# Performance work log

Hardware: AMD Instinct MI355X
Metric: run time of the kernel (lower is better)

The kernel has to match this reference:

```python
import jax, jax.numpy as jnp
import numpy as np

B, C1, C2, K, H, W = 2, 256, 256, 3, 64, 64
PAD = 1
EPS = 1e-5
K2 = K * K
OUT_OFF = 3 * K2  # deform_groups=1: 2*k2 offset channels + k2 mask channels


def setup_inputs() -> dict:
    key = jax.random.key(0)
    ks = jax.random.split(key, 8)
    x = jax.random.normal(ks[0], (B, C1, H, W), jnp.float32)
    # small scale so predicted offsets stay within a few pixels (realistic trained regime)
    w_off = jax.random.normal(ks[1], (OUT_OFF, C1, 3, 3), jnp.float32) * 0.01
    b_off = jax.random.normal(ks[2], (OUT_OFF,), jnp.float32) * 0.01
    w_dcn = jax.random.normal(ks[3], (C2, C1, K, K), jnp.float32) / np.sqrt(C1 * K2).astype(np.float32)
    gamma = 1.0 + 0.1 * jax.random.normal(ks[4], (C2,), jnp.float32)
    beta = 0.1 * jax.random.normal(ks[5], (C2,), jnp.float32)
    run_mean = 0.1 * jax.random.normal(ks[6], (C2,), jnp.float32)
    run_var = jax.random.uniform(ks[7], (C2,), jnp.float32, minval=0.5, maxval=1.5)
    return {"x": x, "w_off": w_off, "b_off": b_off, "w_dcn": w_dcn,
            "gamma": gamma, "beta": beta, "run_mean": run_mean, "run_var": run_var}


def _dcnv2_bn_silu(x, w_off, b_off, w_dcn, gamma, beta, run_mean, run_var):
    # offset/mask predictor: plain 3x3 conv, stride 1, pad 1
    om = jax.lax.conv_general_dilated(x, w_off, (1, 1), [(PAD, PAD), (PAD, PAD)])
    om = om + b_off[None, :, None, None]  # [B, 27, H, W]
    # mmcv channel layout: (dy, dx) interleaved per kernel tap, then mask
    offset = om[:, :2 * K2].reshape(B, K2, 2, H, W)
    mask = jax.nn.sigmoid(om[:, 2 * K2:3 * K2])  # [B, K2, H, W]
    dy, dx = offset[:, :, 0], offset[:, :, 1]     # [B, K2, H, W]

    ki = jnp.arange(K)
    tap_y = jnp.repeat(ki, K)  # [K2]
    tap_x = jnp.tile(ki, K)    # [K2]
    base_y = jnp.arange(H)[None, None, :, None] - PAD + tap_y[None, :, None, None]
    base_x = jnp.arange(W)[None, None, None, :] - PAD + tap_x[None, :, None, None]
    py = base_y.astype(x.dtype) + dy  # [B, K2, H, W] sampling rows
    px = base_x.astype(x.dtype) + dx  # [B, K2, H, W] sampling cols

    y0f = jnp.floor(py)
    x0f = jnp.floor(px)
    ly = (py - y0f)[:, None]  # [B, 1, K2, H, W]
    lx = (px - x0f)[:, None]
    y0 = y0f.astype(jnp.int32)
    x0 = x0f.astype(jnp.int32)

    x_flat = x.reshape(B, C1, H * W)

    def gather(yi, xi):
        valid = ((yi >= 0) & (yi < H) & (xi >= 0) & (xi < W)).astype(x.dtype)
        idx = jnp.clip(yi, 0, H - 1) * W + jnp.clip(xi, 0, W - 1)  # [B, K2, H, W]
        v = jnp.take_along_axis(x_flat, idx.reshape(B, 1, -1), axis=2)
        return v.reshape(B, C1, K2, H, W) * valid[:, None]

    v00 = gather(y0, x0)
    v01 = gather(y0, x0 + 1)
    v10 = gather(y0 + 1, x0)
    v11 = gather(y0 + 1, x0 + 1)
    vals = (v00 * (1 - ly) * (1 - lx) + v01 * (1 - ly) * lx
            + v10 * ly * (1 - lx) + v11 * ly * lx)
    vals = vals * mask[:, None]  # modulated

    out = jnp.einsum('bckhw,ock->bohw', vals, w_dcn.reshape(C2, C1, K2))

    # BatchNorm (inference, running stats) + SiLU
    inv = gamma / jnp.sqrt(run_var + EPS)
    y = out * inv[None, :, None, None] + (beta - run_mean * inv)[None, :, None, None]
    return y * jax.nn.sigmoid(y)


def reference(x, w_off, b_off, w_dcn, gamma, beta, run_mean, run_var):
    return _dcnv2_bn_silu(x, w_off, b_off, w_dcn, gamma, beta, run_mean, run_var)
```

## Files before the change

### kernel.cpp

```cpp
#include <hip/hip_runtime.h>
#include <hip/hip_bf16.h>
#include <math.h>

typedef __bf16 bf16x8 __attribute__((ext_vector_type(8)));
typedef float  f32x4  __attribute__((ext_vector_type(4)));

#define BB 2
#define C1 256
#define C2 256
#define HH 64
#define WW 64
#define HW 4096
#define OCH 27
#define EPSV 1e-5f

#define WBF_OFF  0u
#define WOFF_OFF 1179648u
#define XT_OFF   1327104u

__global__ __launch_bounds__(256) void prep_kernel(
    const float* __restrict__ x, const float* __restrict__ w_dcn,
    const float* __restrict__ w_off, __bf16* __restrict__ xT,
    __bf16* __restrict__ wbfS, __bf16* __restrict__ woffS)
{
    __shared__ __bf16 tile[64][72];
    __shared__ __bf16 lw[16][584];
    const int bi = blockIdx.x, tid = threadIdx.x;

    if (bi < 512) {
        const int b = bi >> 8;
        const int ht = (bi & 255) >> 2;
        const int ct = bi & 3;
        const int hw_l = tid & 63, cg = tid >> 6;
        const float* src = x + ((size_t)(b * 256 + ct * 64 + cg * 16) << 12)
                             + ht * 64 + hw_l;
        #pragma unroll
        for (int i = 0; i < 16; i++)
            tile[hw_l][cg * 16 + i] = (__bf16)src[(size_t)i << 12];
        __syncthreads();
        const int hw_o = tid >> 2, cq = tid & 3;
        __bf16* dst = xT + ((size_t)(b * HW + ht * 64 + hw_o) << 8)
                         + ct * 64 + cq * 16;
        *(bf16x8*)dst       = *(const bf16x8*)&tile[hw_o][cq * 16];
        *(bf16x8*)(dst + 8) = *(const bf16x8*)&tile[hw_o][cq * 16 + 8];
    } else if (bi < 576) {
        const int b2 = bi - 512;
        const int nb = b2 >> 2, qtr = b2 & 3;
        #pragma unroll
        for (int ii = 0; ii < 9; ii++) {
            int m = tid + 256 * ii;
            int base = m * 4;
            int o_l = base / 576;
            int f = base - o_l * 576;
            float4 v = *(const float4*)(w_dcn
                + (size_t)(nb * 16 + o_l) * 2304 + qtr * 576 + f);
            lw[o_l][f]     = (__bf16)v.x;
            lw[o_l][f + 1] = (__bf16)v.y;
            lw[o_l][f + 2] = (__bf16)v.z;
            lw[o_l][f + 3] = (__bf16)v.w;
        }
        __syncthreads();
        for (int p = tid; p < 1152; p += 256) {
            int lane = p & 63, seg = p >> 6;
            int tap = seg >> 1, ks = seg & 1;
            int kb = tap * 4 + qtr;
            int o_l = lane & 15, kq = (lane >> 4) & 3;
            bf16x8 v;
            #pragma unroll
            for (int j = 0; j < 8; j++)
                v[j] = lw[o_l][(ks * 32 + kq * 8 + j) * 9 + tap];
            *(bf16x8*)(wbfS
                + ((size_t)(((kb * 2 + ks) * 16 + nb) * 64 + lane)) * 8) = v;
        }
    } else {
        int t = (bi - 576) * 256 + tid;
        int l = t & 63;
        int nf = (t >> 6) & 1;
        int ks = (t >> 7) & 1;
        int kb = t >> 8;
        int o = nf * 16 + (l & 15);
        int kq = (l >> 4) & 3;
        bf16x8 v;
        #pragma unroll
        for (int j = 0; j < 8; j++) {
            int K = kb * 64 + ks * 32 + kq * 8 + j;
            v[j] = (o < OCH) ? (__bf16)w_off[o * 2304 + (K & 255) * 9 + (K >> 8)]
                             : (__bf16)0.f;
        }
        *(bf16x8*)(woffS + (size_t)t * 8) = v;
    }
}

union SU {
    float sD[4][16][33];
    float sC[2][16][132];
};

__global__ __launch_bounds__(256) void fused_kernel(
    const __bf16* __restrict__ xT, const __bf16* __restrict__ wbfS,
    const __bf16* __restrict__ woffS, const float* __restrict__ b_off,
    const float* __restrict__ gamma, const float* __restrict__ beta,
    const float* __restrict__ rmean, const float* __restrict__ rvar,
    float* __restrict__ out)
{
    __shared__ SU u;
    __shared__ float  sOm[32][16];
    __shared__ int4   sO[9][16];
    __shared__ float4 sW[9][16];

    const int tid = threadIdx.x, wv = tid >> 6, lane = tid & 63;
    const int g = (blockIdx.x & 7) * 64 + (blockIdx.x >> 3);
    const int pixBase = g * 16;
    const int b = pixBase >> 12;
    const int hwBase = pixBase & 4095;
    const int h = hwBase >> 6, w0 = hwBase & 63;
    const int n15 = lane & 15, q4 = lane >> 4;

    const char* xb = (const char*)xT + ((size_t)b << 12) * 512;

    {
        f32x4 acc2[2];
        #pragma unroll
        for (int j = 0; j < 2; j++) acc2[j] = (f32x4){0.f, 0.f, 0.f, 0.f};

        #pragma unroll
        for (int i = 0; i < 9; i++) {
            const int kb = wv * 9 + i;
            const int k = kb >> 2, cc = kb & 3;
            const int kh = k / 3, kw = k % 3;
            const int hh = h + kh - 1;
            const int ww = w0 + n15 + kw - 1;
            const bool valid = (hh >= 0) && (hh < HH) && (ww >= 0) && (ww < WW);
            const int hc = min(max(hh, 0), HH - 1);
            const int wc = min(max(ww, 0), WW - 1);
            const char* src = xb + (size_t)(hc * WW + wc) * 512
                                 + (cc * 64 + q4 * 8) * 2;
            bf16x8 af[2];
            af[0] = *(const bf16x8*)src;
            af[1] = *(const bf16x8*)(src + 64);
            if (!valid) {
                #pragma unroll
                for (int j = 0; j < 8; j++) {
                    af[0][j] = (__bf16)0.f; af[1][j] = (__bf16)0.f;
                }
            }
            #pragma unroll
            for (int nf = 0; nf < 2; nf++) {
                #pragma unroll
                for (int ks = 0; ks < 2; ks++) {
                    bf16x8 bfr = *(const bf16x8*)(woffS
                        + ((size_t)(((kb * 2 + ks) * 2 + nf) * 64 + lane)) * 8);
                    acc2[nf] = __builtin_amdgcn_mfma_f32_16x16x32_bf16(
                        af[ks], bfr, acc2[nf], 0, 0, 0);
                }
            }
        }
        #pragma unroll
        for (int nf = 0; nf < 2; nf++)
            #pragma unroll
            for (int r = 0; r < 4; r++)
                u.sD[wv][q4 * 4 + r][nf * 16 + n15] = acc2[nf][r];
    }
    __syncthreads();
    for (int t = tid; t < OCH * 16; t += 256) {
        int oc = t >> 4, p = t & 15;
        sOm[oc][p] = b_off[oc] + u.sD[0][p][oc] + u.sD[1][p][oc]
                               + u.sD[2][p][oc] + u.sD[3][p][oc];
    }
    __syncthreads();

    if (tid < 144) {
        int k = tid >> 4, p = tid & 15;
        float dy = sOm[2 * k][p];
        float dx = sOm[2 * k + 1][p];
        float mm = sOm[18 + k][p];
        mm = 1.f / (1.f + __expf(-mm));
        float py = (float)(h - 1 + k / 3) + dy;
        float px = (float)(w0 + p - 1 + k % 3) + dx;
        float y0f = floorf(py), x0f = floorf(px);
        float ly = py - y0f, lx = px - x0f;
        int y0 = (int)y0f, x0 = (int)x0f;
        int yc0 = min(max(y0, 0), HH - 1),     yc1 = min(max(y0 + 1, 0), HH - 1);
        int xc0 = min(max(x0, 0), WW - 1),     xc1 = min(max(x0 + 1, 0), WW - 1);
        float vy0 = (y0 >= 0 && y0 < HH) ? 1.f : 0.f;
        float vy1 = (y0 + 1 >= 0 && y0 + 1 < HH) ? 1.f : 0.f;
        float vx0 = (x0 >= 0 && x0 < WW) ? 1.f : 0.f;
        float vx1 = (x0 + 1 >= 0 && x0 + 1 < WW) ? 1.f : 0.f;
        sO[k][p] = (int4){(yc0 * WW + xc0) * 512, (yc0 * WW + xc1) * 512,
                          (yc1 * WW + xc0) * 512, (yc1 * WW + xc1) * 512};
        sW[k][p] = (float4){(1.f - ly) * (1.f - lx) * vy0 * vx0 * mm,
                            (1.f - ly) * lx         * vy0 * vx1 * mm,
                            ly         * (1.f - lx) * vy1 * vx0 * mm,
                            ly         * lx         * vy1 * vx1 * mm};
    }
    __syncthreads();

    f32x4 acc[16];
    #pragma unroll
    for (int j = 0; j < 16; j++) acc[j] = (f32x4){0.f, 0.f, 0.f, 0.f};

    for (int i = 0; i < 9; i++) {
        const int kb = wv * 9 + i;
        const int k = kb >> 2, cc = kb & 3;
        const int4   O = sO[k][n15];
        const float4 W = sW[k][n15];
        const char* base = xb + (cc * 64 + q4 * 8) * 2;

        bf16x8 af[2];
        #pragma unroll
        for (int ks = 0; ks < 2; ks++) {
            const char* bc = base + ks * 64;
            bf16x8 c00 = *(const bf16x8*)(bc + O.x);
            bf16x8 c01 = *(const bf16x8*)(bc + O.y);
            bf16x8 c10 = *(const bf16x8*)(bc + O.z);
            bf16x8 c11 = *(const bf16x8*)(bc + O.w);
            bf16x8 a;
            #pragma unroll
            for (int j = 0; j < 8; j++) {
                float v = W.x * (float)c00[j] + W.y * (float)c01[j]
                        + W.z * (float)c10[j] + W.w * (float)c11[j];
                a[j] = (__bf16)v;
            }
            af[ks] = a;
        }

        #pragma unroll
        for (int half = 0; half < 2; half++) {
            bf16x8 bfr[8][2];
            #pragma unroll
            for (int nb = 0; nb < 8; nb++)
                #pragma unroll
                for (int ks = 0; ks < 2; ks++)
                    bfr[nb][ks] = *(const bf16x8*)(wbfS
                        + ((size_t)(((kb * 2 + ks) * 16 + half * 8 + nb) * 64 + lane)) * 8);
            #pragma unroll
            for (int nb = 0; nb < 8; nb++)
                #pragma unroll
                for (int ks = 0; ks < 2; ks++)
                    acc[half * 8 + nb] = __builtin_amdgcn_mfma_f32_16x16x32_bf16(
                        af[ks], bfr[nb][ks], acc[half * 8 + nb], 0, 0, 0);
        }
    }

    #pragma unroll
    for (int pass = 0; pass < 2; pass++) {
        if (wv < 2) {
            #pragma unroll
            for (int nb = 0; nb < 8; nb++)
                #pragma unroll
                for (int r = 0; r < 4; r++)
                    u.sC[wv][q4 * 4 + r][nb * 16 + n15] = acc[pass * 8 + nb][r];
        }
        __syncthreads();
        if (wv >= 2) {
            #pragma unroll
            for (int nb = 0; nb < 8; nb++)
                #pragma unroll
                for (int r = 0; r < 4; r++)
                    u.sC[wv - 2][q4 * 4 + r][nb * 16 + n15] += acc[pass * 8 + nb][r];
        }
        __syncthreads();

        const int px = tid & 15, og = tid >> 4;
        #pragma unroll
        for (int ii = 0; ii < 8; ii++) {
            int col = og * 8 + ii;
            int o = pass * 128 + col;
            float s = u.sC[0][px][col] + u.sC[1][px][col];
            float inv = gamma[o] * rsqrtf(rvar[o] + EPSV);
            float sh = beta[o] - rmean[o] * inv;
            float y = s * inv + sh;
            out[(size_t)((b * C2 + o) << 12) + hwBase + px]
                = y * (1.f / (1.f + __expf(-y)));
        }
        __syncthreads();
    }
}

extern "C" void kernel_launch(void* const* d_in, const int* in_sizes, int n_in,
                              void* d_out, int out_size, void* d_ws, size_t ws_size,
                              hipStream_t stream) {
    const float* x      = (const float*)d_in[0];
    const float* w_off  = (const float*)d_in[1];
    const float* b_off  = (const float*)d_in[2];
    const float* w_dcn  = (const float*)d_in[3];
    const float* gamma  = (const float*)d_in[4];
    const float* beta   = (const float*)d_in[5];
    const float* rmean  = (const float*)d_in[6];
    const float* rvar   = (const float*)d_in[7];
    float* out = (float*)d_out;

    char* ws = (char*)d_ws;
    __bf16* wbfS  = (__bf16*)(ws + WBF_OFF);
    __bf16* woffS = (__bf16*)(ws + WOFF_OFF);
    __bf16* xT    = (__bf16*)(ws + XT_OFF);

    prep_kernel<<<612, 256, 0, stream>>>(x, w_dcn, w_off, xT, wbfS, woffS);
    fused_kernel<<<512, 256, 0, stream>>>(xT, wbfS, woffS, b_off,
                                          gamma, beta, rmean, rvar, out);
}
```

Before: 121.4 us.

## Split fused DCN kernel K-reduction across eight waves per block

Doubles the block size from 256 to 512 threads. Each of the eight waves now owns one 32-channel K-slice (channel chunk and half) across all nine taps, where before each of four waves owned nine kb slices with both halves. The partial sums of the offset conv and the main GEMM are reduced across eight waves through shared memory, which is enlarged to fit. This halves the serial MFMA and gather chain per wave and adds latency hiding. The costs are a larger LDS footprint, more reduction traffic, and possible register pressure under launch_bounds(512,4).

```diff
diff --git a/kernel.cpp b/kernel.cpp
--- a/kernel.cpp
+++ b/kernel.cpp
@@ -92,11 +92,11 @@
 }
 
 union SU {
-    float sD[4][16][33];
-    float sC[2][16][132];
+    float sD[8][16][33];
+    float sC[4][16][132];
 };
 
-__global__ __launch_bounds__(256) void fused_kernel(
+__global__ __launch_bounds__(512, 4) void fused_kernel(
     const __bf16* __restrict__ xT, const __bf16* __restrict__ wbfS,
     const __bf16* __restrict__ woffS, const float* __restrict__ b_off,
     const float* __restrict__ gamma, const float* __restrict__ beta,
@@ -116,43 +116,37 @@
     const int h = hwBase >> 6, w0 = hwBase & 63;
     const int n15 = lane & 15, q4 = lane >> 4;
 
+    const int cc  = wv >> 1;
+    const int ksw = wv & 1;
     const char* xb = (const char*)xT + ((size_t)b << 12) * 512;
+    const int chOffB = (cc * 64 + ksw * 32 + q4 * 8) * 2;
 
     {
         f32x4 acc2[2];
-        #pragma unroll
-        for (int j = 0; j < 2; j++) acc2[j] = (f32x4){0.f, 0.f, 0.f, 0.f};
-
-        #pragma unroll
-        for (int i = 0; i < 9; i++) {
-            const int kb = wv * 9 + i;
-            const int k = kb >> 2, cc = kb & 3;
+        acc2[0] = (f32x4){0.f, 0.f, 0.f, 0.f};
+        acc2[1] = (f32x4){0.f, 0.f, 0.f, 0.f};
+
+        #pragma unroll
+        for (int k = 0; k < 9; k++) {
+            const int kb = k * 4 + cc;
             const int kh = k / 3, kw = k % 3;
             const int hh = h + kh - 1;
             const int ww = w0 + n15 + kw - 1;
             const bool valid = (hh >= 0) && (hh < HH) && (ww >= 0) && (ww < WW);
             const int hc = min(max(hh, 0), HH - 1);
             const int wc = min(max(ww, 0), WW - 1);
-            const char* src = xb + (size_t)(hc * WW + wc) * 512
-                                 + (cc * 64 + q4 * 8) * 2;
-            bf16x8 af[2];
-            af[0] = *(const bf16x8*)src;
-            af[1] = *(const bf16x8*)(src + 64);
+            bf16x8 af = *(const bf16x8*)(xb + (size_t)(hc * WW + wc) * 512
+                                            + chOffB);
             if (!valid) {
                 #pragma unroll
-                for (int j = 0; j < 8; j++) {
-                    af[0][j] = (__bf16)0.f; af[1][j] = (__bf16)0.f;
-                }
+                for (int j = 0; j < 8; j++) af[j] = (__bf16)0.f;
             }
             #pragma unroll
             for (int nf = 0; nf < 2; nf++) {
-                #pragma unroll
-                for (int ks = 0; ks < 2; ks++) {
-                    bf16x8 bfr = *(const bf16x8*)(woffS
-                        + ((size_t)(((kb * 2 + ks) * 2 + nf) * 64 + lane)) * 8);
-                    acc2[nf] = __builtin_amdgcn_mfma_f32_16x16x32_bf16(
-                        af[ks], bfr, acc2[nf], 0, 0, 0);
-                }
+                bf16x8 bfr = *(const bf16x8*)(woffS
+                    + ((size_t)(((kb * 2 + ksw) * 2 + nf) * 64 + lane)) * 8);
+                acc2[nf] = __builtin_amdgcn_mfma_f32_16x16x32_bf16(
+                    af, bfr, acc2[nf], 0, 0, 0);
             }
         }
         #pragma unroll
@@ -162,10 +156,12 @@
                 u.sD[wv][q4 * 4 + r][nf * 16 + n15] = acc2[nf][r];
     }
     __syncthreads();
-    for (int t = tid; t < OCH * 16; t += 256) {
-        int oc = t >> 4, p = t & 15;
-        sOm[oc][p] = b_off[oc] + u.sD[0][p][oc] + u.sD[1][p][oc]
-                               + u.sD[2][p][oc] + u.sD[3][p][oc];
+    if (tid < OCH * 16) {
+        int oc = tid >> 4, p = tid & 15;
+        float s = b_off[oc];
+        #pragma unroll
+        for (int w = 0; w < 8; w++) s += u.sD[w][p][oc];
+        sOm[oc][p] = s;
     }
     __syncthreads();
 
@@ -199,52 +195,41 @@
     #pragma unroll
     for (int j = 0; j < 16; j++) acc[j] = (f32x4){0.f, 0.f, 0.f, 0.f};
 
-    for (int i = 0; i < 9; i++) {
-        const int kb = wv * 9 + i;
-        const int k = kb >> 2, cc = kb & 3;
+    for (int k = 0; k < 9; k++) {
+        const int kb = k * 4 + cc;
         const int4   O = sO[k][n15];
         const float4 W = sW[k][n15];
-        const char* base = xb + (cc * 64 + q4 * 8) * 2;
-
-        bf16x8 af[2];
-        #pragma unroll
-        for (int ks = 0; ks < 2; ks++) {
-            const char* bc = base + ks * 64;
-            bf16x8 c00 = *(const bf16x8*)(bc + O.x);
-            bf16x8 c01 = *(const bf16x8*)(bc + O.y);
-            bf16x8 c10 = *(const bf16x8*)(bc + O.z);
-            bf16x8 c11 = *(const bf16x8*)(bc + O.w);
-            bf16x8 a;
-            #pragma unroll
-            for (int j = 0; j < 8; j++) {
-                float v = W.x * (float)c00[j] + W.y * (float)c01[j]
-                        + W.z * (float)c10[j] + W.w * (float)c11[j];
-                a[j] = (__bf16)v;
-            }
-            af[ks] = a;
-        }
-
-        #pragma unroll
-        for (int half = 0; half < 2; half++) {
-            bf16x8 bfr[8][2];
-            #pragma unroll
-            for (int nb = 0; nb < 8; nb++)
-                #pragma unroll
-                for (int ks = 0; ks < 2; ks++)
-                    bfr[nb][ks] = *(const bf16x8*)(wbfS
-                        + ((size_t)(((kb * 2 + ks) * 16 + half * 8 + nb) * 64 + lane)) * 8);
-            #pragma unroll
-            for (int nb = 0; nb < 8; nb++)
-                #pragma unroll
-                for (int ks = 0; ks < 2; ks++)
-                    acc[half * 8 + nb] = __builtin_amdgcn_mfma_f32_16x16x32_bf16(
-                        af[ks], bfr[nb][ks], acc[half * 8 + nb], 0, 0, 0);
+        const char* base = xb + chOffB;
+
+        bf16x8 c00 = *(const bf16x8*)(base + O.x);
+        bf16x8 c01 = *(const bf16x8*)(base + O.y);
+        bf16x8 c10 = *(const bf16x8*)(base + O.z);
+        bf16x8 c11 = *(const bf16x8*)(base + O.w);
+        bf16x8 af;
+        #pragma unroll
+        for (int j = 0; j < 8; j++) {
+            float v = W.x * (float)c00[j] + W.y * (float)c01[j]
+                    + W.z * (float)c10[j] + W.w * (float)c11[j];
+            af[j] = (__bf16)v;
+        }
+
+        #pragma unroll
+        for (int hf = 0; hf < 2; hf++) {
+            bf16x8 bfr[8];
+            #pragma unroll
+            for (int nb = 0; nb < 8; nb++)
+                bfr[nb] = *(const bf16x8*)(wbfS
+                    + ((size_t)(((kb * 2 + ksw) * 16 + hf * 8 + nb) * 64 + lane)) * 8);
+            #pragma unroll
+            for (int nb = 0; nb < 8; nb++)
+                acc[hf * 8 + nb] = __builtin_amdgcn_mfma_f32_16x16x32_bf16(
+                    af, bfr[nb], acc[hf * 8 + nb], 0, 0, 0);
         }
     }
 
     #pragma unroll
     for (int pass = 0; pass < 2; pass++) {
-        if (wv < 2) {
+        if (wv < 4) {
             #pragma unroll
             for (int nb = 0; nb < 8; nb++)
                 #pragma unroll
@@ -252,21 +237,22 @@
                     u.sC[wv][q4 * 4 + r][nb * 16 + n15] = acc[pass * 8 + nb][r];
         }
         __syncthreads();
-        if (wv >= 2) {
+        if (wv >= 4) {
             #pragma unroll
             for (int nb = 0; nb < 8; nb++)
                 #pragma unroll
                 for (int r = 0; r < 4; r++)
-                    u.sC[wv - 2][q4 * 4 + r][nb * 16 + n15] += acc[pass * 8 + nb][r];
+                    u.sC[wv - 4][q4 * 4 + r][nb * 16 + n15] += acc[pass * 8 + nb][r];
         }
         __syncthreads();
 
         const int px = tid & 15, og = tid >> 4;
         #pragma unroll
-        for (int ii = 0; ii < 8; ii++) {
-            int col = og * 8 + ii;
+        for (int ii = 0; ii < 4; ii++) {
+            int col = og * 4 + ii;
             int o = pass * 128 + col;
-            float s = u.sC[0][px][col] + u.sC[1][px][col];
+            float s = u.sC[0][px][col] + u.sC[1][px][col]
+                    + u.sC[2][px][col] + u.sC[3][px][col];
             float inv = gamma[o] * rsqrtf(rvar[o] + EPSV);
             float sh = beta[o] - rmean[o] * inv;
             float y = s * inv + sh;
@@ -296,6 +282,6 @@
     __bf16* xT    = (__bf16*)(ws + XT_OFF);
 
     prep_kernel<<<612, 256, 0, stream>>>(x, w_dcn, w_off, xT, wbfS, woffS);
-    fused_kernel<<<512, 256, 0, stream>>>(xT, wbfS, woffS, b_off,
+    fused_kernel<<<512, 512, 0, stream>>>(xT, wbfS, woffS, b_off,
                                           gamma, beta, rmean, rvar, out);
 }
```

Result: no change. 123.0 us (+1.3%).
